# Optimization experiments

Measured on AMD Instinct MI355X. Metric: run time of the kernel, lower is better.

The kernel has to match this reference:

```python
import jax, jax.numpy as jnp
import numpy as np

NUM_HEADS = 16
ROPE_BASE = 10000.0


def _rope_cos_sin(seq_len, head_dim, dtype):
    inv_freq = 1.0 / (ROPE_BASE ** (jnp.arange(0, head_dim, 2, dtype=jnp.float32) / head_dim))
    t = jnp.arange(seq_len, dtype=jnp.float32)
    freqs = t[:, None] * inv_freq[None, :]          # [S, hd/2]
    emb = jnp.concatenate([freqs, freqs], axis=-1)  # [S, hd]
    return jnp.cos(emb).astype(dtype), jnp.sin(emb).astype(dtype)


def _rotate_half(x):
    x1, x2 = jnp.split(x, 2, axis=-1)
    return jnp.concatenate([-x2, x1], axis=-1)


def setup_inputs() -> dict:
    key = jax.random.key(0)
    k1, k2, k3 = jax.random.split(key, 3)
    B, S, D = 4, 2048, 1024
    x = jax.random.normal(k1, (B, S, D), dtype=jnp.float32)
    w_qkv = jax.random.normal(k2, (3 * D, D), dtype=jnp.float32) * (D ** -0.5)
    w_out = jax.random.normal(k3, (D, D), dtype=jnp.float32) * (D ** -0.5)
    return {"x": x, "w_qkv": w_qkv, "w_out": w_out}


def reference(x, w_qkv, w_out):
    B, S, D = x.shape
    H = NUM_HEADS
    hd = D // H
    scale = hd ** -0.5

    qkv = jnp.einsum('bsd,ed->bse', x, w_qkv)           # [B, S, 3D]
    qkv = qkv.reshape(B, S, 3, H, hd).transpose(2, 0, 3, 1, 4)  # [3, B, H, S, hd]
    q, k, v = qkv[0], qkv[1], qkv[2]

    cos, sin = _rope_cos_sin(S, hd, x.dtype)            # [S, hd] broadcast over B,H
    q = q * cos + _rotate_half(q) * sin
    k = k * cos + _rotate_half(k) * sin

    scores = jnp.einsum('bhqd,bhkd->bhqk', q, k) * scale  # [B, H, S, S]
    causal = jnp.tril(jnp.ones((S, S), dtype=bool))
    scores = jnp.where(causal, scores, jnp.finfo(scores.dtype).min)
    attn = jax.nn.softmax(scores, axis=-1)

    out = jnp.einsum('bhqk,bhkd->bhqd', attn, v)        # [B, H, S, hd]
    out = out.transpose(0, 2, 1, 3).reshape(B, S, D)
    out = jnp.einsum('bsd,ed->bse', out, w_out)
    return out
```

## Files before the change

### kernel.cpp

```cpp
#include <hip/hip_runtime.h>
#include <hip/hip_bf16.h>

typedef __bf16 bf16x8 __attribute__((ext_vector_type(8)));
typedef float f32x4 __attribute__((ext_vector_type(4)));
typedef __hip_bfloat16 bf16;

#define B_ 4
#define S_ 2048
#define D_ 1024
#define H_ 16
#define HD_ 64

__device__ __forceinline__ void gload16(const bf16* g, bf16* l) {
  __builtin_amdgcn_global_load_lds(
      (const __attribute__((address_space(1))) unsigned int*)g,
      (__attribute__((address_space(3))) unsigned int*)l, 16, 0, 0);
}

#define NX_ (B_ * S_ * D_)
#define NW1_ (3 * D_ * D_)
#define NW2_ (D_ * D_)
__global__ __launch_bounds__(256) void k_cvt3(const float* __restrict__ x,
                                              const float* __restrict__ w1,
                                              const float* __restrict__ w2,
                                              bf16* __restrict__ ox,
                                              bf16* __restrict__ o1,
                                              bf16* __restrict__ o2) {
  int i = (blockIdx.x * 256 + threadIdx.x) * 4;
  const float* in;
  bf16* out;
  if (i < NX_) {
    in = x; out = ox;
  } else if (i < NX_ + NW1_) {
    in = w1; out = o1; i -= NX_;
  } else {
    in = w2; out = o2; i -= NX_ + NW1_;
  }
  float4 v = *reinterpret_cast<const float4*>(in + i);
  alignas(8) bf16 t[4];
  t[0] = __float2bfloat16(v.x);
  t[1] = __float2bfloat16(v.y);
  t[2] = __float2bfloat16(v.z);
  t[3] = __float2bfloat16(v.w);
  *reinterpret_cast<uint2*>(out + i) = *reinterpret_cast<uint2*>(t);
}

__global__ __launch_bounds__(256) void k_qkv(const bf16* __restrict__ X,
                                             const bf16* __restrict__ W,
                                             bf16* __restrict__ Qw,
                                             bf16* __restrict__ Kw,
                                             bf16* __restrict__ Vtw) {
  __shared__ bf16 Al[128 * 64];
  __shared__ bf16 Bl[128 * 64];
  const int tid = threadIdx.x;
  const int wave = tid >> 6, lane = tid & 63, col = lane & 15, g = lane >> 4;
  const int m0 = blockIdx.x * 128, n0 = blockIdx.y * 128;
  const int wrow = (wave >> 1) * 64, wcol = (wave & 1) * 64;
  const int row8 = tid >> 3;
  const int cel = ((tid & 7) * 8) ^ ((row8 & 7) * 8);
  const bf16* ga = X + (size_t)(m0 + row8) * 1024 + cel;
  const bf16* gb = W + (size_t)(n0 + row8) * 1024 + cel;
  bf16* la = Al + tid * 8;
  bf16* lb = Bl + tid * 8;
  const int rsw = (col & 7) * 8;
  f32x4 acc[4][4] = {};
  for (int k0 = 0; k0 < 1024; k0 += 64) {
    __syncthreads();
#pragma unroll
    for (int i = 0; i < 4; ++i) {
      gload16(ga + k0 + i * 32 * 1024, la + i * 2048);
      gload16(gb + k0 + i * 32 * 1024, lb + i * 2048);
    }
    __syncthreads();
#pragma unroll
    for (int kk = 0; kk < 2; ++kk) {
      const int ce = (kk * 32 + g * 8) ^ rsw;
      bf16x8 af[4], bfr[4];
#pragma unroll
      for (int m = 0; m < 4; ++m)
        af[m] = *reinterpret_cast<const bf16x8*>(&Al[(wrow + m * 16 + col) * 64 + ce]);
#pragma unroll
      for (int n = 0; n < 4; ++n)
        bfr[n] = *reinterpret_cast<const bf16x8*>(&Bl[(wcol + n * 16 + col) * 64 + ce]);
#pragma unroll
      for (int m = 0; m < 4; ++m)
#pragma unroll
        for (int n = 0; n < 4; ++n)
          acc[m][n] =
              __builtin_amdgcn_mfma_f32_16x16x32_bf16(af[m], bfr[n], acc[m][n], 0, 0, 0);
    }
  }
  const int e0 = n0 + wcol;
  const int which = e0 >> 10;
  const int h = (e0 >> 6) & 15;
  if (which == 2) {
#pragma unroll
    for (int m = 0; m < 4; ++m) {
      int mg = m0 + wrow + m * 16 + g * 4;
      int b = mg >> 11, s = mg & 2047;
#pragma unroll
      for (int n = 0; n < 4; ++n) {
        int d = n * 16 + col;
        alignas(8) bf16 t[4];
#pragma unroll
        for (int r = 0; r < 4; ++r) t[r] = __float2bfloat16(acc[m][n][r]);
        *reinterpret_cast<uint2*>(&Vtw[((size_t)((b * 16 + h) * 64 + d) << 11) + s]) =
            *reinterpret_cast<uint2*>(t);
      }
    }
  } else {
    bf16* dst = which ? Kw : Qw;
    const float scale = which ? 1.0f : 0.18033688011112042f;
    const float fexp = -2.0f * 13.287712379549449f / 64.0f;
#pragma unroll
    for (int i = 0; i < 2; ++i) {
      int dlo = i * 16 + col;
      float invf = exp2f(fexp * (float)dlo);
#pragma unroll
      for (int m = 0; m < 4; ++m) {
        int mg = m0 + wrow + m * 16 + g * 4;
        int b = mg >> 11;
        size_t rb = (size_t)(b * 16 + h) << 11;
#pragma unroll
        for (int r = 0; r < 4; ++r) {
          int s = (mg + r) & 2047;
          float sn, cs;
          __sincosf((float)s * invf, &sn, &cs);
          float lo = acc[m][i][r] * scale, hi = acc[m][i + 2][r] * scale;
          dst[((rb + s) << 6) + dlo] = __float2bfloat16(lo * cs - hi * sn);
          dst[((rb + s) << 6) + dlo + 32] = __float2bfloat16(hi * cs + lo * sn);
        }
      }
    }
  }
}

__global__ __launch_bounds__(512) void k_attn(const bf16* __restrict__ Q,
                                              const bf16* __restrict__ K,
                                              const bf16* __restrict__ Vt,
                                              bf16* __restrict__ AO) {
  __shared__ bf16 QPl[128][72];
  __shared__ bf16 Kl[64][72];
  __shared__ bf16 Vl[64][72];
  const int tid = threadIdx.x;
  const int wave = tid >> 6, lane = tid & 63, col = lane & 15, g = lane >> 4;
  const int bh = blockIdx.x;
  const size_t base = (size_t)bh << 17;
  const int r0 = tid >> 3, c0 = (tid & 7) * 8;
  const int b = bh >> 4, h = bh & 15;
  const int yy = blockIdx.y, a = yy >> 2, r_ = yy & 3;
  const int qt = (a == 0) ? (15 - r_) : (a == 1) ? (8 + (r_ ^ 2)) : (a == 2) ? (4 + (r_ ^ 1)) : r_;
  const int q0 = qt * 128;
  *reinterpret_cast<int4*>(&QPl[r0][c0]) =
      *reinterpret_cast<const int4*>(&Q[base + (size_t)(q0 + r0) * 64 + c0]);
  *reinterpret_cast<int4*>(&QPl[r0 + 64][c0]) =
      *reinterpret_cast<const int4*>(&Q[base + (size_t)(q0 + r0 + 64) * 64 + c0]);
  const int ktlim = 2 * qt + 1;
  const int ktmax = (q0 + wave * 16 + 15) >> 6;
  int4 kr = *reinterpret_cast<const int4*>(&K[base + (size_t)r0 * 64 + c0]);
  int4 vr = *reinterpret_cast<const int4*>(&Vt[base + (size_t)r0 * 2048 + c0]);
  *reinterpret_cast<int4*>(&Kl[r0][c0]) = kr;
  *reinterpret_cast<int4*>(&Vl[r0][c0]) = vr;
  kr = *reinterpret_cast<const int4*>(&K[base + (size_t)(64 + r0) * 64 + c0]);
  vr = *reinterpret_cast<const int4*>(&Vt[base + (size_t)r0 * 2048 + 64 + c0]);
  __syncthreads();
  bf16x8 qf[2];
#pragma unroll
  for (int kk = 0; kk < 2; ++kk)
    qf[kk] = *reinterpret_cast<const bf16x8*>(&QPl[wave * 16 + col][g * 8 + kk * 32]);
  float l_s = 0.0f;
  f32x4 o[4] = {};
  for (int kt = 0; kt <= ktlim; ++kt) {
    const int k0 = kt * 64;
    if (kt <= ktmax) {
      const int q = q0 + wave * 16 + col;
      const bool needmask = (k0 + 63 > q0 + wave * 16);
      __builtin_amdgcn_s_setprio(1);
#pragma unroll
      for (int n = 0; n < 4; ++n) {
        f32x4 s = {};
#pragma unroll
        for (int kk = 0; kk < 2; ++kk) {
          bf16x8 kf =
              *reinterpret_cast<const bf16x8*>(&Kl[n * 16 + col][g * 8 + kk * 32]);
          s = __builtin_amdgcn_mfma_f32_16x16x32_bf16(kf, qf[kk], s, 0, 0, 0);
        }
        if (needmask) {
#pragma unroll
          for (int r = 0; r < 4; ++r)
            if (k0 + n * 16 + g * 4 + r > q) s[r] = -3e38f;
        }
        alignas(8) bf16 t[4];
#pragma unroll
        for (int r = 0; r < 4; ++r) {
          float p = exp2f(s[r]);
          l_s += p;
          t[r] = __float2bfloat16(p);
        }
        *reinterpret_cast<uint2*>(&QPl[wave * 16 + col][n * 16 + g * 4]) =
            *reinterpret_cast<uint2*>(t);
      }
#pragma unroll
      for (int kk = 0; kk < 2; ++kk) {
        bf16x8 pf =
            *reinterpret_cast<const bf16x8*>(&QPl[wave * 16 + col][g * 8 + kk * 32]);
#pragma unroll
        for (int n2 = 0; n2 < 4; ++n2) {
          bf16x8 vf =
              *reinterpret_cast<const bf16x8*>(&Vl[n2 * 16 + col][g * 8 + kk * 32]);
          o[n2] = __builtin_amdgcn_mfma_f32_16x16x32_bf16(pf, vf, o[n2], 0, 0, 0);
        }
      }
      __builtin_amdgcn_s_setprio(0);
    }
    __syncthreads();
    if (kt < ktlim) {
      *reinterpret_cast<int4*>(&Kl[r0][c0]) = kr;
      *reinterpret_cast<int4*>(&Vl[r0][c0]) = vr;
      if (kt + 2 <= ktlim) {
        const int k2 = k0 + 128;
        kr = *reinterpret_cast<const int4*>(&K[base + (size_t)(k2 + r0) * 64 + c0]);
        vr = *reinterpret_cast<const int4*>(&Vt[base + (size_t)r0 * 2048 + k2 + c0]);
      }
      __syncthreads();
    }
  }
  l_s += __shfl_xor(l_s, 16);
  l_s += __shfl_xor(l_s, 32);
#pragma unroll
  for (int r = 0; r < 4; ++r) {
    float inv = 1.0f / __shfl(l_s, (lane & 48) | (g * 4 + r));
    int s = q0 + wave * 16 + g * 4 + r;
#pragma unroll
    for (int n2 = 0; n2 < 4; ++n2)
      AO[((size_t)(b * 2048 + s) << 10) + h * 64 + n2 * 16 + col] =
          __float2bfloat16(o[n2][r] * inv);
  }
}

__global__ __launch_bounds__(256) void k_outproj(const bf16* __restrict__ A,
                                                 const bf16* __restrict__ W,
                                                 float* __restrict__ OUT) {
  __shared__ bf16 Al[128 * 64];
  __shared__ bf16 Bl[128 * 64];
  const int tid = threadIdx.x;
  const int wave = tid >> 6, lane = tid & 63, col = lane & 15, g = lane >> 4;
  const int m0 = blockIdx.x * 128, n0 = blockIdx.y * 128;
  const int wrow = (wave >> 1) * 64, wcol = (wave & 1) * 64;
  const int row8 = tid >> 3;
  const int cel = ((tid & 7) * 8) ^ ((row8 & 7) * 8);
  const bf16* ga = A + (size_t)(m0 + row8) * 1024 + cel;
  const bf16* gb = W + (size_t)(n0 + row8) * 1024 + cel;
  bf16* la = Al + tid * 8;
  bf16* lb = Bl + tid * 8;
  const int rsw = (col & 7) * 8;
  f32x4 acc[4][4] = {};
  for (int k0 = 0; k0 < 1024; k0 += 64) {
    __syncthreads();
#pragma unroll
    for (int i = 0; i < 4; ++i) {
      gload16(ga + k0 + i * 32 * 1024, la + i * 2048);
      gload16(gb + k0 + i * 32 * 1024, lb + i * 2048);
    }
    __syncthreads();
#pragma unroll
    for (int kk = 0; kk < 2; ++kk) {
      const int ce = (kk * 32 + g * 8) ^ rsw;
      bf16x8 af[4], bfr[4];
#pragma unroll
      for (int m = 0; m < 4; ++m)
        af[m] = *reinterpret_cast<const bf16x8*>(&Al[(wrow + m * 16 + col) * 64 + ce]);
#pragma unroll
      for (int n = 0; n < 4; ++n)
        bfr[n] = *reinterpret_cast<const bf16x8*>(&Bl[(wcol + n * 16 + col) * 64 + ce]);
#pragma unroll
      for (int m = 0; m < 4; ++m)
#pragma unroll
        for (int n = 0; n < 4; ++n)
          acc[m][n] =
              __builtin_amdgcn_mfma_f32_16x16x32_bf16(af[m], bfr[n], acc[m][n], 0, 0, 0);
    }
  }
#pragma unroll
  for (int m = 0; m < 4; ++m)
#pragma unroll
    for (int n = 0; n < 4; ++n)
#pragma unroll
      for (int r = 0; r < 4; ++r)
        OUT[(size_t)(m0 + wrow + m * 16 + g * 4 + r) * 1024 + n0 + wcol + n * 16 + col] =
            acc[m][n][r];
}

extern "C" void kernel_launch(void* const* d_in, const int* in_sizes, int n_in,
                              void* d_out, int out_size, void* d_ws, size_t ws_size,
                              hipStream_t stream) {
  const float* x = (const float*)d_in[0];
  const float* wqkv = (const float*)d_in[1];
  const float* wout = (const float*)d_in[2];
  float* out = (float*)d_out;

  char* ws = (char*)d_ws;
  const size_t SZ_X = (size_t)B_ * S_ * D_ * 2;
  const size_t SZ_WQKV = (size_t)3 * D_ * D_ * 2;
  const size_t SZ_WOUT = (size_t)D_ * D_ * 2;
  const size_t SZ_T = (size_t)B_ * H_ * S_ * HD_ * 2;
  bf16* xb = (bf16*)(ws);
  bf16* wqkvb = (bf16*)(ws + SZ_X);
  bf16* woutb = (bf16*)(ws + SZ_X + SZ_WQKV);
  bf16* qws = (bf16*)(ws + SZ_X + SZ_WQKV + SZ_WOUT);
  bf16* kws = (bf16*)(ws + SZ_X + SZ_WQKV + SZ_WOUT + SZ_T);
  bf16* vtws = (bf16*)(ws + SZ_X + SZ_WQKV + SZ_WOUT + 2 * SZ_T);
  bf16* aob = (bf16*)(ws + SZ_X + SZ_WQKV + SZ_WOUT + 3 * SZ_T);

  const int NTOT4 = (NX_ + NW1_ + NW2_) / 4;
  k_cvt3<<<NTOT4 / 256, 256, 0, stream>>>(x, wqkv, wout, xb, wqkvb, woutb);

  k_qkv<<<dim3(64, 24), 256, 0, stream>>>(xb, wqkvb, qws, kws, vtws);
  k_attn<<<dim3(B_ * H_, 16), 512, 0, stream>>>(qws, kws, vtws, aob);
  k_outproj<<<dim3(64, 8), 256, 0, stream>>>(aob, woutb, out);
}
```

Before: 162.7 us.

## Double-buffer LDS and widen GEMM tiles to 128x256 in QKV and out-projection

Rewrites both projection GEMMs to use 512-thread blocks with 128x256 output tiles and two LDS buffers. Global loads for tile k+2 are issued asynchronously while tile k is computed, with vmcnt waits replacing the full syncthreads pair, and MFMA sections get raised wave priority. The aim is to hide global-to-LDS latency and get more reuse of the A tile. In exchange, LDS use triples to 96KB per block and the grid is halved (768 and 256 blocks), which can reduce occupancy and leave the out-projection grid short of filling all CUs.

```diff
diff --git a/kernel.cpp b/kernel.cpp
--- a/kernel.cpp
+++ b/kernel.cpp
@@ -45,58 +45,76 @@
   *reinterpret_cast<uint2*>(out + i) = *reinterpret_cast<uint2*>(t);
 }
 
-__global__ __launch_bounds__(256) void k_qkv(const bf16* __restrict__ X,
+__global__ __launch_bounds__(512) void k_qkv(const bf16* __restrict__ X,
                                              const bf16* __restrict__ W,
                                              bf16* __restrict__ Qw,
                                              bf16* __restrict__ Kw,
                                              bf16* __restrict__ Vtw) {
-  __shared__ bf16 Al[128 * 64];
-  __shared__ bf16 Bl[128 * 64];
+  __shared__ bf16 Al[2][128 * 64];
+  __shared__ bf16 Bl[2][256 * 64];
   const int tid = threadIdx.x;
-  const int wave = tid >> 6, lane = tid & 63, col = lane & 15, g = lane >> 4;
-  const int m0 = blockIdx.x * 128, n0 = blockIdx.y * 128;
-  const int wrow = (wave >> 1) * 64, wcol = (wave & 1) * 64;
-  const int row8 = tid >> 3;
-  const int cel = ((tid & 7) * 8) ^ ((row8 & 7) * 8);
-  const bf16* ga = X + (size_t)(m0 + row8) * 1024 + cel;
-  const bf16* gb = W + (size_t)(n0 + row8) * 1024 + cel;
-  bf16* la = Al + tid * 8;
-  bf16* lb = Bl + tid * 8;
+  const int wid = tid >> 6, lane = tid & 63, col = lane & 15, g = lane >> 4;
+  const int wr = wid >> 2, wc = wid & 3;
+  const int m0 = blockIdx.x * 128, n0 = blockIdx.y * 256;
+  const int srow = tid >> 3;
+  const int scol = (tid & 7) * 8;
+  const int csrc = scol ^ ((srow & 7) * 8);
+  const bf16* ga = X + (size_t)(m0 + srow) * 1024 + csrc;
+  const bf16* gb = W + (size_t)(n0 + srow) * 1024 + csrc;
+  const int ldst = srow * 64 + scol;
   const int rsw = (col & 7) * 8;
   f32x4 acc[4][4] = {};
-  for (int k0 = 0; k0 < 1024; k0 += 64) {
-    __syncthreads();
-#pragma unroll
-    for (int i = 0; i < 4; ++i) {
-      gload16(ga + k0 + i * 32 * 1024, la + i * 2048);
-      gload16(gb + k0 + i * 32 * 1024, lb + i * 2048);
-    }
-    __syncthreads();
+#define QKV_STAGE(buf, k0)                                   \
+  do {                                                       \
+    gload16(ga + (k0), &Al[buf][ldst]);                      \
+    gload16(ga + (k0) + 64 * 1024, &Al[buf][ldst + 4096]);   \
+    gload16(gb + (k0), &Bl[buf][ldst]);                      \
+    gload16(gb + (k0) + 64 * 1024, &Bl[buf][ldst + 4096]);   \
+    gload16(gb + (k0) + 128 * 1024, &Bl[buf][ldst + 8192]);  \
+    gload16(gb + (k0) + 192 * 1024, &Bl[buf][ldst + 12288]); \
+  } while (0)
+  QKV_STAGE(0, 0);
+  QKV_STAGE(1, 64);
+  for (int kt = 0; kt < 16; ++kt) {
+    const int c = kt & 1;
+    if (kt < 15)
+      asm volatile("s_waitcnt vmcnt(6)" ::: "memory");
+    else
+      asm volatile("s_waitcnt vmcnt(0)" ::: "memory");
+    __builtin_amdgcn_s_barrier();
+    const bf16* Ac = Al[c];
+    const bf16* Bc = Bl[c];
 #pragma unroll
     for (int kk = 0; kk < 2; ++kk) {
       const int ce = (kk * 32 + g * 8) ^ rsw;
       bf16x8 af[4], bfr[4];
 #pragma unroll
       for (int m = 0; m < 4; ++m)
-        af[m] = *reinterpret_cast<const bf16x8*>(&Al[(wrow + m * 16 + col) * 64 + ce]);
+        af[m] = *reinterpret_cast<const bf16x8*>(&Ac[(wr * 64 + m * 16 + col) * 64 + ce]);
 #pragma unroll
       for (int n = 0; n < 4; ++n)
-        bfr[n] = *reinterpret_cast<const bf16x8*>(&Bl[(wcol + n * 16 + col) * 64 + ce]);
+        bfr[n] =
+            *reinterpret_cast<const bf16x8*>(&Bc[(wc * 64 + n * 16 + col) * 64 + ce]);
+      __builtin_amdgcn_s_setprio(1);
 #pragma unroll
       for (int m = 0; m < 4; ++m)
 #pragma unroll
         for (int n = 0; n < 4; ++n)
           acc[m][n] =
               __builtin_amdgcn_mfma_f32_16x16x32_bf16(af[m], bfr[n], acc[m][n], 0, 0, 0);
-    }
-  }
-  const int e0 = n0 + wcol;
+      __builtin_amdgcn_s_setprio(0);
+    }
+    __builtin_amdgcn_s_barrier();
+    if (kt + 2 < 16) QKV_STAGE(c, (kt + 2) * 64);
+  }
+#undef QKV_STAGE
+  const int e0 = n0 + wc * 64;
   const int which = e0 >> 10;
   const int h = (e0 >> 6) & 15;
   if (which == 2) {
 #pragma unroll
     for (int m = 0; m < 4; ++m) {
-      int mg = m0 + wrow + m * 16 + g * 4;
+      int mg = m0 + wr * 64 + m * 16 + g * 4;
       int b = mg >> 11, s = mg & 2047;
 #pragma unroll
       for (int n = 0; n < 4; ++n) {
@@ -118,7 +136,7 @@
       float invf = exp2f(fexp * (float)dlo);
 #pragma unroll
       for (int m = 0; m < 4; ++m) {
-        int mg = m0 + wrow + m * 16 + g * 4;
+        int mg = m0 + wr * 64 + m * 16 + g * 4;
         int b = mg >> 11;
         size_t rb = (size_t)(b * 16 + h) << 11;
 #pragma unroll
@@ -238,57 +256,75 @@
   }
 }
 
-__global__ __launch_bounds__(256) void k_outproj(const bf16* __restrict__ A,
+__global__ __launch_bounds__(512) void k_outproj(const bf16* __restrict__ A,
                                                  const bf16* __restrict__ W,
                                                  float* __restrict__ OUT) {
-  __shared__ bf16 Al[128 * 64];
-  __shared__ bf16 Bl[128 * 64];
+  __shared__ bf16 Al[2][128 * 64];
+  __shared__ bf16 Bl[2][256 * 64];
   const int tid = threadIdx.x;
-  const int wave = tid >> 6, lane = tid & 63, col = lane & 15, g = lane >> 4;
-  const int m0 = blockIdx.x * 128, n0 = blockIdx.y * 128;
-  const int wrow = (wave >> 1) * 64, wcol = (wave & 1) * 64;
-  const int row8 = tid >> 3;
-  const int cel = ((tid & 7) * 8) ^ ((row8 & 7) * 8);
-  const bf16* ga = A + (size_t)(m0 + row8) * 1024 + cel;
-  const bf16* gb = W + (size_t)(n0 + row8) * 1024 + cel;
-  bf16* la = Al + tid * 8;
-  bf16* lb = Bl + tid * 8;
+  const int wid = tid >> 6, lane = tid & 63, col = lane & 15, g = lane >> 4;
+  const int wr = wid >> 2, wc = wid & 3;
+  const int m0 = blockIdx.x * 128, n0 = blockIdx.y * 256;
+  const int srow = tid >> 3;
+  const int scol = (tid & 7) * 8;
+  const int csrc = scol ^ ((srow & 7) * 8);
+  const bf16* ga = A + (size_t)(m0 + srow) * 1024 + csrc;
+  const bf16* gb = W + (size_t)(n0 + srow) * 1024 + csrc;
+  const int ldst = srow * 64 + scol;
   const int rsw = (col & 7) * 8;
   f32x4 acc[4][4] = {};
-  for (int k0 = 0; k0 < 1024; k0 += 64) {
-    __syncthreads();
-#pragma unroll
-    for (int i = 0; i < 4; ++i) {
-      gload16(ga + k0 + i * 32 * 1024, la + i * 2048);
-      gload16(gb + k0 + i * 32 * 1024, lb + i * 2048);
-    }
-    __syncthreads();
+#define OP_STAGE(buf, k0)                                    \
+  do {                                                       \
+    gload16(ga + (k0), &Al[buf][ldst]);                      \
+    gload16(ga + (k0) + 64 * 1024, &Al[buf][ldst + 4096]);   \
+    gload16(gb + (k0), &Bl[buf][ldst]);                      \
+    gload16(gb + (k0) + 64 * 1024, &Bl[buf][ldst + 4096]);   \
+    gload16(gb + (k0) + 128 * 1024, &Bl[buf][ldst + 8192]);  \
+    gload16(gb + (k0) + 192 * 1024, &Bl[buf][ldst + 12288]); \
+  } while (0)
+  OP_STAGE(0, 0);
+  OP_STAGE(1, 64);
+  for (int kt = 0; kt < 16; ++kt) {
+    const int c = kt & 1;
+    if (kt < 15)
+      asm volatile("s_waitcnt vmcnt(6)" ::: "memory");
+    else
+      asm volatile("s_waitcnt vmcnt(0)" ::: "memory");
+    __builtin_amdgcn_s_barrier();
+    const bf16* Ac = Al[c];
+    const bf16* Bc = Bl[c];
 #pragma unroll
     for (int kk = 0; kk < 2; ++kk) {
       const int ce = (kk * 32 + g * 8) ^ rsw;
       bf16x8 af[4], bfr[4];
 #pragma unroll
       for (int m = 0; m < 4; ++m)
-        af[m] = *reinterpret_cast<const bf16x8*>(&Al[(wrow + m * 16 + col) * 64 + ce]);
+        af[m] = *reinterpret_cast<const bf16x8*>(&Ac[(wr * 64 + m * 16 + col) * 64 + ce]);
 #pragma unroll
       for (int n = 0; n < 4; ++n)
-        bfr[n] = *reinterpret_cast<const bf16x8*>(&Bl[(wcol + n * 16 + col) * 64 + ce]);
+        bfr[n] =
+            *reinterpret_cast<const bf16x8*>(&Bc[(wc * 64 + n * 16 + col) * 64 + ce]);
+      __builtin_amdgcn_s_setprio(1);
 #pragma unroll
       for (int m = 0; m < 4; ++m)
 #pragma unroll
         for (int n = 0; n < 4; ++n)
           acc[m][n] =
               __builtin_amdgcn_mfma_f32_16x16x32_bf16(af[m], bfr[n], acc[m][n], 0, 0, 0);
-    }
-  }
+      __builtin_amdgcn_s_setprio(0);
+    }
+    __builtin_amdgcn_s_barrier();
+    if (kt + 2 < 16) OP_STAGE(c, (kt + 2) * 64);
+  }
+#undef OP_STAGE
 #pragma unroll
   for (int m = 0; m < 4; ++m)
 #pragma unroll
     for (int n = 0; n < 4; ++n)
 #pragma unroll
       for (int r = 0; r < 4; ++r)
-        OUT[(size_t)(m0 + wrow + m * 16 + g * 4 + r) * 1024 + n0 + wcol + n * 16 + col] =
-            acc[m][n][r];
+        OUT[(size_t)(m0 + wr * 64 + m * 16 + g * 4 + r) * 1024 + n0 + wc * 64 + n * 16 +
+            col] = acc[m][n][r];
 }
 
 extern "C" void kernel_launch(void* const* d_in, const int* in_sizes, int n_in,
@@ -315,7 +351,7 @@
   const int NTOT4 = (NX_ + NW1_ + NW2_) / 4;
   k_cvt3<<<NTOT4 / 256, 256, 0, stream>>>(x, wqkv, wout, xb, wqkvb, woutb);
 
-  k_qkv<<<dim3(64, 24), 256, 0, stream>>>(xb, wqkvb, qws, kws, vtws);
+  k_qkv<<<dim3(64, 12), 512, 0, stream>>>(xb, wqkvb, qws, kws, vtws);
   k_attn<<<dim3(B_ * H_, 16), 512, 0, stream>>>(qws, kws, vtws, aob);
-  k_outproj<<<dim3(64, 8), 256, 0, stream>>>(aob, woutb, out);
-}
+  k_outproj<<<dim3(64, 4), 512, 0, stream>>>(aob, woutb, out);
+}
```

After: 176.3 us. 8.3% more time.
